# Performance work log

Measured on AMD Instinct MI355X. Metric: run time of the kernel, lower is better.

Reference implementation:

```python
import jax, jax.numpy as jnp
import numpy as np

N, E = 100000, 3200000
IN, HID, OUT, EDGE = 32, 32, 32, 8

def _lin(k, fi, fo):
    s = 1.0 / np.sqrt(fi)
    return jax.random.uniform(k, (fi, fo), jnp.float32, -s, s)

def setup_inputs() -> dict:
    key = jax.random.key(0)
    ks = jax.random.split(key, 12)
    return {
        "node_feat": jax.random.normal(ks[0], (N, IN), jnp.float32),
        "coord_feat": jax.random.normal(ks[1], (N, 3), jnp.float32),
        "edge_feat": jax.random.normal(ks[2], (E, EDGE), jnp.float32),
        "src": jax.random.randint(ks[3], (E,), 0, N, jnp.int32),
        "dst": jax.random.randint(ks[4], (E,), 0, N, jnp.int32),
        # edge MLP: Linear(2*IN+EDGE+1 -> HID), SiLU, Linear(HID -> HID), SiLU
        "We1": _lin(ks[5], 2 * IN + EDGE + 1, HID), "be1": jnp.zeros((HID,), jnp.float32),
        "We2": _lin(ks[6], HID, HID), "be2": jnp.zeros((HID,), jnp.float32),
        # node MLP: Linear(IN+HID -> HID), SiLU, Linear(HID -> OUT)
        "Wn1": _lin(ks[7], IN + HID, HID), "bn1": jnp.zeros((HID,), jnp.float32),
        "Wn2": _lin(ks[8], HID, OUT), "bn2": jnp.zeros((OUT,), jnp.float32),
        # coord MLP: Linear(HID -> HID), SiLU, Linear(HID -> 1, bias=False)
        "Wc1": _lin(ks[9], HID, HID), "bc1": jnp.zeros((HID,), jnp.float32),
        "Wc2": _lin(ks[10], HID, 1),
    }

def reference(node_feat, coord_feat, edge_feat, src, dst,
              We1, be1, We2, be2, Wn1, bn1, Wn2, bn2, Wc1, bc1, Wc2):
    silu = jax.nn.silu
    # per-edge coordinate difference and radial feature (DGL EGNNConv math)
    x_diff = coord_feat[src] - coord_feat[dst]                       # [E,3]
    radial = jnp.sum(x_diff * x_diff, axis=-1, keepdims=True)        # [E,1]
    x_diff = x_diff / (jnp.sqrt(radial) + 1e-30)                     # normalized
    # edge MLP on concat(src_h, dst_h, radial, edge_feat)
    f = jnp.concatenate([node_feat[src], node_feat[dst], radial, edge_feat], axis=-1)
    msg_h = silu(silu(f @ We1 + be1) @ We2 + be2)                    # [E,HID]
    # coordinate message (coord MLP scalar gate * normalized diff)
    msg_x = (silu(msg_h @ Wc1 + bc1) @ Wc2) * x_diff                 # [E,3]
    # aggregate: sum for h messages, mean for coord messages (at dst)
    h_neigh = jax.ops.segment_sum(msg_h, dst, num_segments=N)        # [N,HID]
    deg = jax.ops.segment_sum(jnp.ones((E, 1), msg_x.dtype), dst, num_segments=N)
    x_neigh = jax.ops.segment_sum(msg_x, dst, num_segments=N) / jnp.maximum(deg, 1.0)
    # node update
    h = silu(jnp.concatenate([node_feat, h_neigh], axis=-1) @ Wn1 + bn1) @ Wn2 + bn2
    x = coord_feat + x_neigh
    return h, x
```

## Files before the change

### kernel.cpp

```cpp
#include <hip/hip_runtime.h>
#include <math.h>

#define TIN   32
#define THID  32
#define TOUT  32
#define TEDGE 8
#define CHUNK 4
#define MAXDEG 64

typedef __attribute__((ext_vector_type(8))) short bf16x8;
typedef __attribute__((ext_vector_type(4))) float f32x4;

#define MFMA16(a, b, c) __builtin_amdgcn_mfma_f32_16x16x32_bf16((a), (b), (c), 0, 0, 0)

__device__ __forceinline__ unsigned int cvtpk(float lo, float hi) {
    unsigned int r;
    asm("v_cvt_pk_bf16_f32 %0, %1, %2" : "=v"(r) : "v"(lo), "v"(hi));
    return r;
}

__device__ __forceinline__ float silu_f(float x) {
    float e = __expf(-x);
    return x * __builtin_amdgcn_rcpf(1.0f + e);
}

__device__ __forceinline__ float bflo(unsigned int u) { return __uint_as_float(u << 16); }
__device__ __forceinline__ float bfhi(unsigned int u) { return __uint_as_float(u & 0xFFFF0000u); }

union U4F { unsigned int u[4]; bf16x8 v; };
union U4Q { uint4 q; bf16x8 v; };

__device__ __forceinline__ bf16x8 pack8bf(const float* f) {
    U4F t;
    t.u[0] = cvtpk(f[0], f[1]);
    t.u[1] = cvtpk(f[2], f[3]);
    t.u[2] = cvtpk(f[4], f[5]);
    t.u[3] = cvtpk(f[6], f[7]);
    return t.v;
}

__device__ __forceinline__ bf16x8 load_wT(const float* __restrict__ W, int kbase, int ch, int Kreal) {
    float f[8];
    #pragma unroll
    for (int e = 0; e < 8; ++e) {
        int k = kbase + e;
        f[e] = (k < Kreal) ? W[k * 32 + ch] : 0.0f;
    }
    return pack8bf(f);
}

__device__ __forceinline__ bf16x8 load_wA12(const float* __restrict__ We1,
                                            const float* __restrict__ be1, int g, int ch) {
    float f[8];
    #pragma unroll
    for (int e = 0; e < 8; ++e) f[e] = 0.0f;
    if (g == 0) { f[0] = We1[72 * 32 + ch]; f[1] = be1[ch]; }
    else if (g == 1) {
        #pragma unroll
        for (int e = 0; e < 8; ++e) f[e] = We1[(64 + e) * 32 + ch];
    }
    return pack8bf(f);
}

__global__ __launch_bounds__(256) void conv_node_kernel(
    const float* __restrict__ nf, unsigned int* __restrict__ nb, int total )
{
    int i = blockIdx.x * 256 + threadIdx.x;
    int stride = gridDim.x * 256;
    for (; i < total; i += stride) {
        float2 v = reinterpret_cast<const float2*>(nf)[i];
        nb[i] = cvtpk(v.x, v.y);
    }
}

__global__ __launch_bounds__(256) void conv_coord_kernel(
    const float* __restrict__ c, float4* __restrict__ c4, int N)
{
    int i = blockIdx.x * 256 + threadIdx.x;
    int stride = gridDim.x * 256;
    for (; i < N; i += stride) {
        float4 v;
        v.x = c[3*(size_t)i+0]; v.y = c[3*(size_t)i+1]; v.z = c[3*(size_t)i+2]; v.w = 0.0f;
        c4[i] = v;
    }
}

__global__ __launch_bounds__(256) void record_rank_kernel(
    const int* __restrict__ src,
    const int* __restrict__ dst,
    const float4* __restrict__ coord4,
    const float* __restrict__ edge_feat,
    int* __restrict__ cnt,
    uint4* __restrict__ recs,
    int E)
{
    int e = blockIdx.x * 256 + threadIdx.x;
    if (e >= E) return;
    int s = src[e], d = dst[e];
    int rank = atomicAdd(&cnt[d], 1);
    if (rank >= MAXDEG) return;

    float4 cs = coord4[s];
    float4 cd = coord4[d];
    float dx0 = cs.x - cd.x, dx1 = cs.y - cd.y, dx2 = cs.z - cd.z;
    float radial = dx0*dx0 + dx1*dx1 + dx2*dx2;
    float invn = __builtin_amdgcn_rcpf(sqrtf(radial) + 1e-30f);
    dx0 *= invn; dx1 *= invn; dx2 *= invn;

    const float4* ep = reinterpret_cast<const float4*>(edge_feat + (size_t)e * TEDGE);
    float4 e0 = ep[0], e1 = ep[1];

    size_t slot = ((size_t)d << 6) + rank;
    uint4 r0, r1;
    r0.x = (unsigned int)s;
    r0.y = cvtpk(dx0, dx1);
    r0.z = cvtpk(dx2, e1.w);
    r0.w = 0u;
    r1.x = cvtpk(radial, e0.x);
    r1.y = cvtpk(e0.y, e0.z);
    r1.z = cvtpk(e0.w, e1.x);
    r1.w = cvtpk(e1.y, e1.z);
    recs[2*slot + 0] = r0;
    recs[2*slot + 1] = r1;
}

__global__ __launch_bounds__(256) void egnn_fused(
    const uint4* __restrict__ node_bf4,
    const uint4* __restrict__ recs,
    const int*  __restrict__ cnt,
    const float* __restrict__ We1,
    const float* __restrict__ be1,
    const float* __restrict__ We2,
    const float* __restrict__ be2,
    const float* __restrict__ Wc1,
    const float* __restrict__ bc1,
    const float* __restrict__ Wc2,
    float4* __restrict__ h_acc4,
    float4* __restrict__ xd4,
    int N)
{
    const int lane = threadIdx.x & 63;
    const int wid  = threadIdx.x >> 6;
    const int r    = lane & 15;
    const int g    = lane >> 4;

    bf16x8 A10[2], A11[2], A12[2], A2[2], A3[2];
    A10[0] = load_wT(We1,      8*g, r,      73);
    A10[1] = load_wT(We1,      8*g, 16 + r, 73);
    A11[0] = load_wT(We1, 32 + 8*g, r,      73);
    A11[1] = load_wT(We1, 32 + 8*g, 16 + r, 73);
    A12[0] = load_wA12(We1, be1, g, r);
    A12[1] = load_wA12(We1, be1, g, 16 + r);
    A2[0] = load_wT(We2, 8*g, r, 32);      A2[1] = load_wT(We2, 8*g, 16 + r, 32);
    A3[0] = load_wT(Wc1, 8*g, r, 32);      A3[1] = load_wT(Wc1, 8*g, 16 + r, 32);

    float be2v[8], bc1v[8], wc2v[8];
    #pragma unroll
    for (int h = 0; h < 2; ++h)
        #pragma unroll
        for (int q = 0; q < 4; ++q) {
            int ch = 16*h + 4*g + q;
            be2v[4*h+q] = be2[ch];
            bc1v[4*h+q] = bc1[ch];
            wc2v[4*h+q] = Wc2[ch];
        }

    const bool Hhi = ((g >> 1) & 1) != 0;
    const int  s0L = 32 * (g & 1) + r;
    const int  s1L = s0L + 16;

    int c0n = (blockIdx.x * 4 + wid) * CHUNK;

    for (int n = c0n; n < c0n + CHUNK && n < N; ++n) {
        int deg = cnt[n];
        int len = deg < MAXDEG ? deg : MAXDEG;
        size_t segbase = ((size_t)n << 6);

        U4Q Bd; Bd.q = node_bf4[(size_t)n * 4 + g];

        f32x4 z4 = {0.f,0.f,0.f,0.f};
        f32x4 dst0 = MFMA16(A11[0], Bd.v, z4);
        f32x4 dst1 = MFMA16(A11[1], Bd.v, z4);

        float ha0[4] = {0.f,0.f,0.f,0.f}, ha1[4] = {0.f,0.f,0.f,0.f};
        float xa0 = 0.f, xa1 = 0.f, xa2 = 0.f;

        for (int t = 0; t < len; t += 16) {
            int idx = t + r;
            bool valid = idx < len;
            size_t slot = segbase + (valid ? idx : 0);

            uint4 rc = recs[2*slot + (g & 1)];
            int srcv = __shfl((int)rc.x, r, 64);

            U4Q Bs; Bs.q = node_bf4[(size_t)srcv * 4 + g];

            U4F Bk2;
            Bk2.u[0] = 0u; Bk2.u[1] = 0u; Bk2.u[2] = 0u; Bk2.u[3] = 0u;
            if (g == 0) {
                Bk2.u[0] = (rc.z >> 16) | 0x3F800000u;
            } else if (g == 1) {
                Bk2.u[0] = rc.x; Bk2.u[1] = rc.y; Bk2.u[2] = rc.z; Bk2.u[3] = rc.w;
            }

            f32x4 acc0 = dst0, acc1 = dst1;
            acc0 = MFMA16(A10[0], Bs.v,   acc0);
            acc0 = MFMA16(A12[0], Bk2.v,  acc0);
            acc1 = MFMA16(A10[1], Bs.v,   acc1);
            acc1 = MFMA16(A12[1], Bk2.v,  acc1);

            unsigned int pk0 = cvtpk(silu_f(acc0[0]), silu_f(acc0[1]));
            unsigned int pk1 = cvtpk(silu_f(acc0[2]), silu_f(acc0[3]));
            unsigned int pk2 = cvtpk(silu_f(acc1[0]), silu_f(acc1[1]));
            unsigned int pk3 = cvtpk(silu_f(acc1[2]), silu_f(acc1[3]));

            unsigned int al0 = __shfl(pk0, s0L, 64), al1 = __shfl(pk1, s0L, 64);
            unsigned int ah0 = __shfl(pk2, s0L, 64), ah1 = __shfl(pk3, s0L, 64);
            unsigned int bl0 = __shfl(pk0, s1L, 64), bl1 = __shfl(pk1, s1L, 64);
            unsigned int bh0 = __shfl(pk2, s1L, 64), bh1 = __shfl(pk3, s1L, 64);
            U4F B2u;
            B2u.u[0] = Hhi ? ah0 : al0;  B2u.u[1] = Hhi ? ah1 : al1;
            B2u.u[2] = Hhi ? bh0 : bl0;  B2u.u[3] = Hhi ? bh1 : bl1;

            f32x4 m0, m1;
            #pragma unroll
            for (int q = 0; q < 4; ++q) { m0[q] = be2v[q]; m1[q] = be2v[4+q]; }
            m0 = MFMA16(A2[0], B2u.v, m0);
            m1 = MFMA16(A2[1], B2u.v, m1);

            float vm = valid ? 1.0f : 0.0f;
            float s00 = silu_f(m0[0]) * vm, s01 = silu_f(m0[1]) * vm;
            float s02 = silu_f(m0[2]) * vm, s03 = silu_f(m0[3]) * vm;
            float s10 = silu_f(m1[0]) * vm, s11 = silu_f(m1[1]) * vm;
            float s12 = silu_f(m1[2]) * vm, s13 = silu_f(m1[3]) * vm;

            ha0[0] += s00; ha0[1] += s01; ha0[2] += s02; ha0[3] += s03;
            ha1[0] += s10; ha1[1] += s11; ha1[2] += s12; ha1[3] += s13;

            unsigned int mpk0 = cvtpk(s00, s01);
            unsigned int mpk1 = cvtpk(s02, s03);
            unsigned int mpk2 = cvtpk(s10, s11);
            unsigned int mpk3 = cvtpk(s12, s13);

            unsigned int cl0 = __shfl(mpk0, s0L, 64), cl1 = __shfl(mpk1, s0L, 64);
            unsigned int ch0 = __shfl(mpk2, s0L, 64), ch1 = __shfl(mpk3, s0L, 64);
            unsigned int dl0 = __shfl(mpk0, s1L, 64), dl1 = __shfl(mpk1, s1L, 64);
            unsigned int dh0 = __shfl(mpk2, s1L, 64), dh1 = __shfl(mpk3, s1L, 64);
            U4F B3u;
            B3u.u[0] = Hhi ? ch0 : cl0;  B3u.u[1] = Hhi ? ch1 : cl1;
            B3u.u[2] = Hhi ? dh0 : dl0;  B3u.u[3] = Hhi ? dh1 : dl1;

            f32x4 c0, c1;
            #pragma unroll
            for (int q = 0; q < 4; ++q) { c0[q] = bc1v[q]; c1[q] = bc1v[4+q]; }
            c0 = MFMA16(A3[0], B3u.v, c0);
            c1 = MFMA16(A3[1], B3u.v, c1);

            float gp = 0.0f;
            #pragma unroll
            for (int q = 0; q < 4; ++q) {
                gp = fmaf(silu_f(c0[q]), wc2v[q],   gp);
                gp = fmaf(silu_f(c1[q]), wc2v[4+q], gp);
            }
            gp += __shfl_xor(gp, 16, 64);
            gp += __shfl_xor(gp, 32, 64);

            float xd0 = bflo(rc.y), xd1 = bfhi(rc.y), xd2 = bflo(rc.z);
            xa0 = fmaf(gp * vm, xd0, xa0);
            xa1 = fmaf(gp * vm, xd1, xa1);
            xa2 = fmaf(gp * vm, xd2, xa2);
        }

        #pragma unroll
        for (int off = 1; off < 16; off <<= 1) {
            #pragma unroll
            for (int q = 0; q < 4; ++q) {
                ha0[q] += __shfl_xor(ha0[q], off, 64);
                ha1[q] += __shfl_xor(ha1[q], off, 64);
            }
            xa0 += __shfl_xor(xa0, off, 64);
            xa1 += __shfl_xor(xa1, off, 64);
            xa2 += __shfl_xor(xa2, off, 64);
        }

        if (r == 0) {
            float4 v0; v0.x = ha0[0]; v0.y = ha0[1]; v0.z = ha0[2]; v0.w = ha0[3];
            float4 v1; v1.x = ha1[0]; v1.y = ha1[1]; v1.z = ha1[2]; v1.w = ha1[3];
            h_acc4[(size_t)n * 8 + g]     = v0;
            h_acc4[(size_t)n * 8 + 4 + g] = v1;
            if (g == 0) {
                float4 xv; xv.x = xa0; xv.y = xa1; xv.z = xa2; xv.w = (float)deg;
                xd4[n] = xv;
            }
        }
    }
}

__global__ __launch_bounds__(256) void ovf_fix_node(
    const float* __restrict__ node_feat,
    const float* __restrict__ coord,
    const float* __restrict__ edge_feat,
    const int* __restrict__ src,
    const int* __restrict__ dst,
    const int* __restrict__ cnt,
    const float* __restrict__ We1,
    const float* __restrict__ be1,
    const float* __restrict__ We2,
    const float* __restrict__ be2,
    const float* __restrict__ Wc1,
    const float* __restrict__ bc1,
    const float* __restrict__ Wc2,
    float* __restrict__ h_acc,
    float4* __restrict__ xd4,
    int N, int E)
{
    int n = blockIdx.x * 256 + threadIdx.x;
    if (n >= N) return;
    if (cnt[n] <= MAXDEG) return;

    float hsum[THID];
    #pragma unroll
    for (int j = 0; j < THID; ++j) hsum[j] = 0.f;
    float xs0 = 0.f, xs1 = 0.f, xs2 = 0.f;
    int degc = 0;
    for (int ee = 0; ee < E; ++ee) {
        if (dst[ee] != n) continue;
        ++degc;
        int ss = src[ee];
        float dx0 = coord[3*(size_t)ss+0] - coord[3*(size_t)n+0];
        float dx1 = coord[3*(size_t)ss+1] - coord[3*(size_t)n+1];
        float dx2 = coord[3*(size_t)ss+2] - coord[3*(size_t)n+2];
        float radial = dx0*dx0 + dx1*dx1 + dx2*dx2;
        float invn = 1.0f / (sqrtf(radial) + 1e-30f);
        dx0 *= invn; dx1 *= invn; dx2 *= invn;
        float f[73];
        for (int k = 0; k < 32; ++k) f[k] = node_feat[(size_t)ss*TIN + k];
        for (int k = 0; k < 32; ++k) f[32+k] = node_feat[(size_t)n*TIN + k];
        f[64] = radial;
        for (int k = 0; k < 8; ++k) f[65+k] = edge_feat[(size_t)ee*TEDGE + k];
        float a1[THID];
        for (int j = 0; j < THID; ++j) a1[j] = be1[j];
        for (int k = 0; k < 73; ++k) {
            float fk = f[k];
            for (int j = 0; j < THID; ++j) a1[j] = fmaf(fk, We1[k*THID + j], a1[j]);
        }
        for (int j = 0; j < THID; ++j) a1[j] = silu_f(a1[j]);
        float msg[THID];
        for (int j = 0; j < THID; ++j) msg[j] = be2[j];
        for (int k = 0; k < THID; ++k) {
            float fk = a1[k];
            for (int j = 0; j < THID; ++j) msg[j] = fmaf(fk, We2[k*THID + j], msg[j]);
        }
        for (int j = 0; j < THID; ++j) msg[j] = silu_f(msg[j]);
        float c1[THID];
        for (int j = 0; j < THID; ++j) c1[j] = bc1[j];
        for (int k = 0; k < THID; ++k) {
            float fk = msg[k];
            for (int j = 0; j < THID; ++j) c1[j] = fmaf(fk, Wc1[k*THID + j], c1[j]);
        }
        float gate = 0.0f;
        for (int j = 0; j < THID; ++j) gate = fmaf(silu_f(c1[j]), Wc2[j], gate);
        for (int j = 0; j < THID; ++j) hsum[j] += msg[j];
        xs0 += gate * dx0; xs1 += gate * dx1; xs2 += gate * dx2;
    }
    for (int j = 0; j < THID; ++j) h_acc[(size_t)n * THID + j] = hsum[j];
    float4 xv; xv.x = xs0; xv.y = xs1; xv.z = xs2; xv.w = (float)degc;
    xd4[n] = xv;
}

__global__ __launch_bounds__(256) void egnn_edge_atomic(
    const float* __restrict__ node_feat,
    const float* __restrict__ coord,
    const float* __restrict__ edge_feat,
    const int*   __restrict__ src,
    const int*   __restrict__ dst,
    const float* __restrict__ We1,
    const float* __restrict__ be1,
    const float* __restrict__ We2,
    const float* __restrict__ be2,
    const float* __restrict__ Wc1,
    const float* __restrict__ bc1,
    const float* __restrict__ Wc2,
    float* __restrict__ h_acc,
    float* __restrict__ x_acc,
    int E)
{
    int e = blockIdx.x * 256 + threadIdx.x;
    if (e >= E) return;
    int s = src[e];
    int d = dst[e];
    float dx0 = coord[3*(size_t)s+0] - coord[3*(size_t)d+0];
    float dx1 = coord[3*(size_t)s+1] - coord[3*(size_t)d+1];
    float dx2 = coord[3*(size_t)s+2] - coord[3*(size_t)d+2];
    float radial = dx0*dx0 + dx1*dx1 + dx2*dx2;
    float invn = 1.0f / (sqrtf(radial) + 1e-30f);
    dx0 *= invn; dx1 *= invn; dx2 *= invn;
    float f[73];
    #pragma unroll
    for (int i = 0; i < 32; ++i) f[i] = node_feat[(size_t)s*TIN + i];
    #pragma unroll
    for (int i = 0; i < 32; ++i) f[32+i] = node_feat[(size_t)d*TIN + i];
    f[64] = radial;
    #pragma unroll
    for (int i = 0; i < 8; ++i) f[65+i] = edge_feat[(size_t)e*TEDGE + i];
    float a1[THID];
    #pragma unroll
    for (int j = 0; j < THID; ++j) a1[j] = be1[j];
    for (int k = 0; k < 73; ++k) {
        float fk = f[k];
        #pragma unroll
        for (int j = 0; j < THID; ++j) a1[j] = fmaf(fk, We1[k*THID + j], a1[j]);
    }
    #pragma unroll
    for (int j = 0; j < THID; ++j) a1[j] = silu_f(a1[j]);
    float msg[THID];
    #pragma unroll
    for (int j = 0; j < THID; ++j) msg[j] = be2[j];
    for (int k = 0; k < THID; ++k) {
        float fk = a1[k];
        #pragma unroll
        for (int j = 0; j < THID; ++j) msg[j] = fmaf(fk, We2[k*THID + j], msg[j]);
    }
    #pragma unroll
    for (int j = 0; j < THID; ++j) msg[j] = silu_f(msg[j]);
    float c1[THID];
    #pragma unroll
    for (int j = 0; j < THID; ++j) c1[j] = bc1[j];
    for (int k = 0; k < THID; ++k) {
        float fk = msg[k];
        #pragma unroll
        for (int j = 0; j < THID; ++j) c1[j] = fmaf(fk, Wc1[k*THID + j], c1[j]);
    }
    float gate = 0.0f;
    #pragma unroll
    for (int j = 0; j < THID; ++j) gate = fmaf(silu_f(c1[j]), Wc2[j], gate);
    float* ha = h_acc + (size_t)d * THID;
    #pragma unroll
    for (int j = 0; j < THID; ++j) atomicAdd(ha + j, msg[j]);
    atomicAdd(x_acc + (size_t)d*4 + 0, gate * dx0);
    atomicAdd(x_acc + (size_t)d*4 + 1, gate * dx1);
    atomicAdd(x_acc + (size_t)d*4 + 2, gate * dx2);
    atomicAdd(x_acc + (size_t)d*4 + 3, 1.0f);
}

__global__ __launch_bounds__(256) void egnn_node(
    const float* __restrict__ node_feat,
    const float* __restrict__ coord,
    const float* __restrict__ Wn1,
    const float* __restrict__ bn1,
    const float* __restrict__ Wn2,
    const float* __restrict__ bn2,
    const float* __restrict__ h_acc,
    const float4* __restrict__ xd4,
    float* __restrict__ out_h,
    float* __restrict__ out_x,
    int N)
{
    int n = blockIdx.x * 256 + threadIdx.x;
    if (n >= N) return;

    float f2[2*TIN];
    {
        const float4* p = reinterpret_cast<const float4*>(node_feat + (size_t)n * TIN);
        #pragma unroll
        for (int i = 0; i < TIN/4; ++i) {
            float4 v = p[i];
            f2[4*i+0]=v.x; f2[4*i+1]=v.y; f2[4*i+2]=v.z; f2[4*i+3]=v.w;
        }
    }
    {
        const float4* p = reinterpret_cast<const float4*>(h_acc + (size_t)n * THID);
        #pragma unroll
        for (int i = 0; i < THID/4; ++i) {
            float4 v = p[i];
            f2[TIN+4*i+0]=v.x; f2[TIN+4*i+1]=v.y; f2[TIN+4*i+2]=v.z; f2[TIN+4*i+3]=v.w;
        }
    }

    float a[THID];
    #pragma unroll
    for (int j = 0; j < THID; ++j) a[j] = bn1[j];
    #pragma unroll
    for (int k = 0; k < 2*TIN; ++k) {
        float fk = f2[k];
        #pragma unroll
        for (int j = 0; j < THID; ++j) a[j] = fmaf(fk, Wn1[k*THID + j], a[j]);
    }
    #pragma unroll
    for (int j = 0; j < THID; ++j) a[j] = silu_f(a[j]);

    float h[TOUT];
    #pragma unroll
    for (int j = 0; j < TOUT; ++j) h[j] = bn2[j];
    #pragma unroll
    for (int k = 0; k < THID; ++k) {
        float fk = a[k];
        #pragma unroll
        for (int j = 0; j < TOUT; ++j) h[j] = fmaf(fk, Wn2[k*TOUT + j], h[j]);
    }

    float4* po = reinterpret_cast<float4*>(out_h + (size_t)n * TOUT);
    #pragma unroll
    for (int i = 0; i < TOUT/4; ++i) {
        float4 v; v.x=h[4*i+0]; v.y=h[4*i+1]; v.z=h[4*i+2]; v.w=h[4*i+3];
        po[i] = v;
    }

    float4 xv = xd4[n];
    float dg = fmaxf(xv.w, 1.0f);
    float inv = __builtin_amdgcn_rcpf(dg);
    out_x[(size_t)n*3+0] = coord[(size_t)n*3+0] + xv.x * inv;
    out_x[(size_t)n*3+1] = coord[(size_t)n*3+1] + xv.y * inv;
    out_x[(size_t)n*3+2] = coord[(size_t)n*3+2] + xv.z * inv;
}

extern "C" void kernel_launch(void* const* d_in, const int* in_sizes, int n_in,
                              void* d_out, int out_size, void* d_ws, size_t ws_size,
                              hipStream_t stream) {
    const float* node_feat = (const float*)d_in[0];
    const float* coord     = (const float*)d_in[1];
    const float* edge_feat = (const float*)d_in[2];
    const int*   src       = (const int*)d_in[3];
    const int*   dst       = (const int*)d_in[4];
    const float* We1 = (const float*)d_in[5];
    const float* be1 = (const float*)d_in[6];
    const float* We2 = (const float*)d_in[7];
    const float* be2 = (const float*)d_in[8];
    const float* Wn1 = (const float*)d_in[9];
    const float* bn1 = (const float*)d_in[10];
    const float* Wn2 = (const float*)d_in[11];
    const float* bn2 = (const float*)d_in[12];
    const float* Wc1 = (const float*)d_in[13];
    const float* bc1 = (const float*)d_in[14];
    const float* Wc2 = (const float*)d_in[15];

    int N = in_sizes[0] / TIN;
    int E = in_sizes[3];

    float* out_h = (float*)d_out;
    float* out_x = out_h + (size_t)N * TOUT;

    uint4*        recs    = (uint4*)d_ws;
    unsigned int* node_bf = (unsigned int*)(recs + ((size_t)N << 6) * 2);
    float4*       coord4  = (float4*)(node_bf + (size_t)N * 16);
    float*        h_acc   = (float*)(coord4 + N);
    float4*       xd4     = (float4*)(h_acc + (size_t)N * THID);
    int*          cnt     = (int*)(xd4 + N);
    size_t need = (size_t)((char*)(cnt + N + 1) - (char*)d_ws);

    if (need <= ws_size) {
        conv_node_kernel<<<2048, 256, 0, stream>>>(node_feat, node_bf, N * 16);
        conv_coord_kernel<<<(N + 255) / 256, 256, 0, stream>>>(coord, coord4, N);
        hipMemsetAsync(cnt, 0, (size_t)(N + 1) * 4, stream);
        record_rank_kernel<<<(E + 255) / 256, 256, 0, stream>>>(
            src, dst, coord4, edge_feat, cnt, recs, E);
        int nchunks = (N + CHUNK - 1) / CHUNK;
        egnn_fused<<<(nchunks + 3) / 4, 256, 0, stream>>>(
            (const uint4*)node_bf, recs, cnt,
            We1, be1, We2, be2, Wc1, bc1, Wc2,
            (float4*)h_acc, xd4, N);
        ovf_fix_node<<<(N + 255) / 256, 256, 0, stream>>>(
            node_feat, coord, edge_feat, src, dst, cnt,
            We1, be1, We2, be2, Wc1, bc1, Wc2, h_acc, xd4, N, E);
        egnn_node<<<(N + 255) / 256, 256, 0, stream>>>(
            node_feat, coord, Wn1, bn1, Wn2, bn2,
            h_acc, xd4, out_h, out_x, N);
    } else {
        float* fh_acc = (float*)d_ws;
        float* fx_acc = fh_acc + (size_t)N * THID;
        hipMemsetAsync(d_ws, 0, sizeof(float) * (size_t)N * (THID + 4), stream);
        egnn_edge_atomic<<<(E + 255) / 256, 256, 0, stream>>>(
            node_feat, coord, edge_feat, src, dst,
            We1, be1, We2, be2, Wc1, bc1, Wc2,
            fh_acc, fx_acc, E);
        egnn_node<<<(N + 255) / 256, 256, 0, stream>>>(
            node_feat, coord, Wn1, bn1, Wn2, bn2,
            fh_acc, (const float4*)fx_acc, out_h, out_x, N);
    }
}
```

Before: 476.4 us.

## Prefetch next edge batch in fused loop and merge prep kernels

The fused edge kernel now software-pipelines its per-node edge loop. It loads the next 16-edge record and the gathered source node features before computing the current batch, to hide gather latency behind the MFMA and SiLU work. It also merges the node bf16 conversion, the coord padding and the count memset into one prep kernel, cutting two launches. The prefetch adds register pressure, which may lower occupancy.

```diff
diff --git a/kernel.cpp b/kernel.cpp
--- a/kernel.cpp
+++ b/kernel.cpp
@@ -62,27 +62,24 @@
     return pack8bf(f);
 }
 
-__global__ __launch_bounds__(256) void conv_node_kernel(
-    const float* __restrict__ nf, unsigned int* __restrict__ nb, int total )
+__global__ __launch_bounds__(256) void prep_kernel(
+    const float* __restrict__ nf, const float* __restrict__ c,
+    unsigned int* __restrict__ nb, float4* __restrict__ c4,
+    int* __restrict__ cnt, int N)
 {
     int i = blockIdx.x * 256 + threadIdx.x;
     int stride = gridDim.x * 256;
-    for (; i < total; i += stride) {
-        float2 v = reinterpret_cast<const float2*>(nf)[i];
-        nb[i] = cvtpk(v.x, v.y);
-    }
-}
-
-__global__ __launch_bounds__(256) void conv_coord_kernel(
-    const float* __restrict__ c, float4* __restrict__ c4, int N)
-{
-    int i = blockIdx.x * 256 + threadIdx.x;
-    int stride = gridDim.x * 256;
-    for (; i < N; i += stride) {
+    int total = N * 16;
+    for (int j = i; j < total; j += stride) {
+        float2 v = reinterpret_cast<const float2*>(nf)[j];
+        nb[j] = cvtpk(v.x, v.y);
+    }
+    for (int j = i; j < N; j += stride) {
         float4 v;
-        v.x = c[3*(size_t)i+0]; v.y = c[3*(size_t)i+1]; v.z = c[3*(size_t)i+2]; v.w = 0.0f;
-        c4[i] = v;
-    }
+        v.x = c[3*(size_t)j+0]; v.y = c[3*(size_t)j+1]; v.z = c[3*(size_t)j+2]; v.w = 0.0f;
+        c4[j] = v;
+    }
+    for (int j = i; j <= N; j += stride) cnt[j] = 0;
 }
 
 __global__ __launch_bounds__(256) void record_rank_kernel(
@@ -185,15 +182,28 @@
         float ha0[4] = {0.f,0.f,0.f,0.f}, ha1[4] = {0.f,0.f,0.f,0.f};
         float xa0 = 0.f, xa1 = 0.f, xa2 = 0.f;
 
+        uint4 rc_cur; rc_cur.x = 0u; rc_cur.y = 0u; rc_cur.z = 0u; rc_cur.w = 0u;
+        U4Q Bs_cur; Bs_cur.q.x = 0u; Bs_cur.q.y = 0u; Bs_cur.q.z = 0u; Bs_cur.q.w = 0u;
+        if (len > 0) {
+            size_t slot0 = segbase + ((r < len) ? r : 0);
+            rc_cur = recs[2*slot0 + (g & 1)];
+            int srcv0 = __shfl((int)rc_cur.x, r, 64);
+            Bs_cur.q = node_bf4[(size_t)srcv0 * 4 + g];
+        }
+
         for (int t = 0; t < len; t += 16) {
             int idx = t + r;
             bool valid = idx < len;
-            size_t slot = segbase + (valid ? idx : 0);
-
-            uint4 rc = recs[2*slot + (g & 1)];
-            int srcv = __shfl((int)rc.x, r, 64);
-
-            U4Q Bs; Bs.q = node_bf4[(size_t)srcv * 4 + g];
+            uint4 rc = rc_cur;
+            U4Q Bs = Bs_cur;
+
+            if (t + 16 < len) {
+                int idx2 = t + 16 + r;
+                size_t slot2 = segbase + ((idx2 < len) ? (size_t)idx2 : 0);
+                rc_cur = recs[2*slot2 + (g & 1)];
+                int srcv2 = __shfl((int)rc_cur.x, r, 64);
+                Bs_cur.q = node_bf4[(size_t)srcv2 * 4 + g];
+            }
 
             U4F Bk2;
             Bk2.u[0] = 0u; Bk2.u[1] = 0u; Bk2.u[2] = 0u; Bk2.u[3] = 0u;
@@ -549,9 +559,7 @@
     size_t need = (size_t)((char*)(cnt + N + 1) - (char*)d_ws);
 
     if (need <= ws_size) {
-        conv_node_kernel<<<2048, 256, 0, stream>>>(node_feat, node_bf, N * 16);
-        conv_coord_kernel<<<(N + 255) / 256, 256, 0, stream>>>(coord, coord4, N);
-        hipMemsetAsync(cnt, 0, (size_t)(N + 1) * 4, stream);
+        prep_kernel<<<2048, 256, 0, stream>>>(node_feat, coord, node_bf, coord4, cnt, N);
         record_rank_kernel<<<(E + 255) / 256, 256, 0, stream>>>(
             src, dst, coord4, edge_feat, cnt, recs, E);
         int nchunks = (N + CHUNK - 1) / CHUNK;
```

After: 463.8 us (median of 2 runs). -2.6%, faster.
